# Kernel tuning notes

Measured on AMD Instinct MI355X. Metric: run time of the kernel, lower is better.

Reference implementation:

```python
import jax, jax.numpy as jnp
import numpy as np

D_MODEL = 4096
N_TYPES = 6  # fixed event_types list in the module


def setup_inputs() -> dict:
    key = jax.random.key(0)
    ks = jax.random.split(key, 7)
    E, B, d = 131072, 16384, D_MODEL
    return {
        "event_type": jax.random.randint(ks[0], (E,), 0, N_TYPES),
        "confidence": jax.random.uniform(ks[1], (E,), jnp.float32),
        "location": jax.random.uniform(ks[2], (E, 2), jnp.float32) * jnp.array([640.0, 480.0], jnp.float32),
        "batch_idx": jax.random.randint(ks[3], (E,), 0, B),
        "batch_size": B,
        "type_emb": jax.random.normal(ks[4], (N_TYPES, d // 4), jnp.float32),
        "W1": jax.random.normal(ks[5], (d // 2, d // 4 + 3), jnp.float32) / np.sqrt(d // 4 + 3).astype(np.float32),
        "b1": jnp.zeros((d // 2,), jnp.float32),
        "W2": jax.random.normal(ks[6], (d, d // 2), jnp.float32) / np.sqrt(d // 2).astype(np.float32),
        "b2": jnp.zeros((d,), jnp.float32),
    }


def reference(event_type, confidence, location, batch_idx, batch_size, type_emb, W1, b1, W2, b2):
    E = confidence.shape[0]
    B = batch_size
    # per-batch-slot max confidence (empty slots -> -inf)
    seg_max = jax.ops.segment_max(confidence, batch_idx, num_segments=B)
    is_top = confidence == seg_max[batch_idx]
    # first event attaining the max (matches torch's max-over-list semantics)
    cand = jnp.where(is_top, jnp.arange(E), E)
    top_idx = jnp.full((B,), E, dtype=cand.dtype).at[batch_idx].min(cand)
    has_event = top_idx < E
    safe_idx = jnp.where(has_event, top_idx, 0)

    emb = type_emb[event_type[safe_idx]]                 # [B, d/4]
    c = confidence[safe_idx][:, None]                    # [B, 1]
    loc = location[safe_idx] / jnp.array([640.0, 480.0], jnp.float32)  # [B, 2]
    feats = jnp.concatenate([emb, c, loc], axis=-1)      # [B, d/4 + 3]

    h = jax.nn.relu(feats @ W1.T + b1)                   # [B, d/2]
    out = h @ W2.T + b2                                  # [B, d]
    return jnp.where(has_event[:, None], out, jnp.zeros((), out.dtype))
```

## Files before the change

kernel.cpp:

```cpp
#include <hip/hip_runtime.h>
#include <hip/hip_bf16.h>

#define NT 6
#define BM 256
#define BN 256
#define BK 64
#define SLOT_S 32768
#define AH1 8192
#define BH0 16384
#define BH1 24576

typedef __attribute__((ext_vector_type(4))) float f32x4;
typedef __attribute__((ext_vector_type(8))) short bf16x8;

__device__ __forceinline__ short f2bf(float f) {
    __hip_bfloat16 h = __float2bfloat16(f);
    return (short)__builtin_bit_cast(unsigned short, h);
}

__global__ void k_segmax(const float* __restrict__ conf,
                         const int* __restrict__ bidx,
                         unsigned long long* __restrict__ packed, int E) {
    int i = blockIdx.x * blockDim.x + threadIdx.x;
    if (i >= E) return;
    unsigned cb = __float_as_uint(conf[i]);
    unsigned long long p = ((unsigned long long)cb << 32) | (unsigned)(~(unsigned)i);
    atomicMax(&packed[bidx[i]], p);
}

__global__ void k_base(const float* __restrict__ emb, const float* __restrict__ W1,
                       const float* __restrict__ b1, float* __restrict__ base,
                       float* __restrict__ vecs, int d2, int d4) {
    int gw = (blockIdx.x * blockDim.x + threadIdx.x) >> 6;
    int lane = threadIdx.x & 63;
    int t = gw / d2, n = gw % d2;
    const float* e = emb + (size_t)t * d4;
    const float* w = W1 + (size_t)n * (d4 + 3);
    float s = 0.f;
    for (int k = lane; k < d4; k += 64) s += e[k] * w[k];
#pragma unroll
    for (int m = 32; m; m >>= 1) s += __shfl_xor(s, m);
    if (lane == 0) {
        base[gw] = s + b1[n];
        if (t == 0) {
            vecs[n]          = w[d4];
            vecs[d2 + n]     = w[d4 + 1];
            vecs[2 * d2 + n] = w[d4 + 2];
        }
    }
}

__global__ void k_w2cast(const float* __restrict__ W2, short* __restrict__ W2b, long n) {
    long i = ((long)blockIdx.x * blockDim.x + threadIdx.x) * 8;
    if (i >= n) return;
    bf16x8 v;
#pragma unroll
    for (int j = 0; j < 8; ++j) v[j] = f2bf(W2[i + j]);
    *(bf16x8*)(W2b + i) = v;
}

__global__ void k_h(const unsigned long long* __restrict__ packed,
                    const int* __restrict__ etype, const float* __restrict__ loc,
                    const float* __restrict__ base, const float* __restrict__ vecs,
                    float* __restrict__ mask, short* __restrict__ h, int d2) {
    int b = blockIdx.x;
    int tid = threadIdx.x;
    unsigned long long p = packed[b];
    bool has = (p != 0ULL);
    float conf = 0.f, lx = 0.f, ly = 0.f;
    int t = 0;
    if (has) {
        unsigned idx = ~(unsigned)(p & 0xFFFFFFFFu);
        conf = __uint_as_float((unsigned)(p >> 32));
        t  = etype[idx];
        lx = loc[2 * (size_t)idx]     * (1.0f / 640.0f);
        ly = loc[2 * (size_t)idx + 1] * (1.0f / 480.0f);
    }
    if (tid == 0) mask[b] = has ? 1.0f : 0.0f;
    const float* bs = base + (size_t)t * d2;
    const float* cv = vecs;
    const float* xv = vecs + d2;
    const float* yv = vecs + 2 * d2;
    int n0 = tid * 8;
    bf16x8 v;
#pragma unroll
    for (int j = 0; j < 8; ++j) {
        int n = n0 + j;
        float g = bs[n] + conf * cv[n] + lx * xv[n] + ly * yv[n];
        g = fmaxf(g, 0.f);
        v[j] = has ? f2bf(g) : (short)0;
    }
    *(bf16x8*)(h + (size_t)b * d2 + n0) = v;
}


#define GLL(src, dst) __builtin_amdgcn_global_load_lds(                      \
    (const __attribute__((address_space(1))) void*)(src),                    \
    (__attribute__((address_space(3))) void*)(dst), 16, 0, 0)

#define ST_AH0(ws, kt) { GLL(pA + (size_t)(kt) * 64, (ws) + dst1);           \
                         GLL(pA + (size_t)64 * K + (kt) * 64, (ws) + dst2); }
#define ST_AH1(ws, kt) { GLL(pA + (size_t)128 * K + (kt) * 64, (ws) + AH1 + dst1); \
                         GLL(pA + (size_t)192 * K + (kt) * 64, (ws) + AH1 + dst2); }
#define ST_BH0(ws, kt) { GLL(pB + (size_t)(kt) * 64, (ws) + BH0 + dst1);     \
                         GLL(pB + (size_t)64 * K + (kt) * 64, (ws) + BH0 + dst2); }
#define ST_BH1(ws, kt) { GLL(pB + (size_t)128 * K + (kt) * 64, (ws) + BH1 + dst1); \
                         GLL(pB + (size_t)192 * K + (kt) * 64, (ws) + BH1 + dst2); }

__global__ __launch_bounds__(512, 2)
void k_gemm(const short* __restrict__ A, const short* __restrict__ Bm,
            const float* __restrict__ b2, const float* __restrict__ mask,
            float* __restrict__ C, int M, int N, int K, int nbn) {
    __shared__ __align__(16) short lds[2 * SLOT_S];

    int tid = threadIdx.x;
    int lane = tid & 63;
    int wave = tid >> 6;
    int wr = wave >> 2, wc = wave & 3;

    int bid = blockIdx.x;
    int wg = (bid & 7) * ((int)gridDim.x >> 3) + (bid >> 3);
    int bm = wg / nbn, bn = wg % nbn;
    int row0 = bm * BM, col0 = bn * BN;

    int r1 = tid >> 3;
    int pg = tid & 7;
    int cg = pg ^ (r1 & 7);
    const short* pA = A + (size_t)(row0 + r1) * K + cg * 8;
    const short* pB = Bm + (size_t)(col0 + r1) * K + cg * 8;
    int dst1 = tid * 8;
    int dst2 = 4096 + tid * 8;

    int frow = lane & 15, fk = lane >> 4;
    int kx = frow & 7;
    int aoffs0 = (wr * 64 + frow) * 64 + ((fk) ^ kx) * 8;
    int aoffs1 = (wr * 64 + frow) * 64 + ((4 + fk) ^ kx) * 8;
    int boffs0 = (wc * 32 + frow) * 64 + ((fk) ^ kx) * 8;
    int boffs1 = (wc * 32 + frow) * 64 + ((4 + fk) ^ kx) * 8;

    f32x4 acc[8][4] = {};
    bf16x8 aA[8][2], bB[4][2];

    int KT = K / BK;

    ST_AH0(lds, 0); ST_BH0(lds, 0); ST_BH1(lds, 0); ST_AH1(lds, 0);
    asm volatile("s_waitcnt vmcnt(0)" ::: "memory");
    __builtin_amdgcn_s_barrier();

#pragma unroll 1
    for (int t = 0; t < KT; ++t) {
        const short* sl = lds + (t & 1) * SLOT_S;
        short* wsl = lds + ((t + 1) & 1) * SLOT_S;

#pragma unroll
        for (int m = 0; m < 4; ++m) {
            aA[m][0]     = *(const bf16x8*)(sl + aoffs0 + m * 1024);
            aA[m][1]     = *(const bf16x8*)(sl + aoffs1 + m * 1024);
        }
#pragma unroll
        for (int n = 0; n < 2; ++n) {
            bB[n][0]     = *(const bf16x8*)(sl + BH0 + boffs0 + n * 1024);
            bB[n][1]     = *(const bf16x8*)(sl + BH0 + boffs1 + n * 1024);
            bB[2 + n][0] = *(const bf16x8*)(sl + BH1 + boffs0 + n * 1024);
            bB[2 + n][1] = *(const bf16x8*)(sl + BH1 + boffs1 + n * 1024);
        }
#pragma unroll
        for (int m = 0; m < 4; ++m) {
            aA[4 + m][0] = *(const bf16x8*)(sl + AH1 + aoffs0 + m * 1024);
            aA[4 + m][1] = *(const bf16x8*)(sl + AH1 + aoffs1 + m * 1024);
        }

        if (t < KT - 1) {
            ST_AH0(wsl, t + 1); ST_BH0(wsl, t + 1);
            ST_BH1(wsl, t + 1); ST_AH1(wsl, t + 1);
        }

        __builtin_amdgcn_s_setprio(1);
#pragma unroll
        for (int m = 0; m < 8; ++m)
#pragma unroll
            for (int n = 0; n < 4; ++n) {
                acc[m][n] = __builtin_amdgcn_mfma_f32_16x16x32_bf16(
                    aA[m][0], bB[n][0], acc[m][n], 0, 0, 0);
                acc[m][n] = __builtin_amdgcn_mfma_f32_16x16x32_bf16(
                    aA[m][1], bB[n][1], acc[m][n], 0, 0, 0);
            }
        __builtin_amdgcn_s_setprio(0);

        if (t < KT - 1) {
            asm volatile("s_waitcnt vmcnt(0)" ::: "memory");
            __builtin_amdgcn_s_barrier();
        }
    }

#pragma unroll
    for (int mi = 0; mi < 8; ++mi) {
        int rbase = row0 + (mi >> 2) * 128 + wr * 64 + (mi & 3) * 16 + fk * 4;
#pragma unroll
        for (int j = 0; j < 4; ++j) {
            int r = rbase + j;
            float mk = mask[r];
#pragma unroll
            for (int ni = 0; ni < 4; ++ni) {
                int cc = col0 + (ni >> 1) * 128 + wc * 32 + (ni & 1) * 16 + frow;
                C[(size_t)r * N + cc] = (acc[mi][ni][j] + b2[cc]) * mk;
            }
        }
    }
}

extern "C" void kernel_launch(void* const* d_in, const int* in_sizes, int n_in,
                              void* d_out, int out_size, void* d_ws, size_t ws_size,
                              hipStream_t stream) {
    const int* etype   = (const int*)d_in[0];
    const float* conf  = (const float*)d_in[1];
    const float* loc   = (const float*)d_in[2];
    const int* bidx    = (const int*)d_in[3];
    const float* emb   = (const float*)d_in[5];
    const float* W1    = (const float*)d_in[6];
    const float* b1    = (const float*)d_in[7];
    const float* W2    = (const float*)d_in[8];
    const float* b2    = (const float*)d_in[9];
    float* out = (float*)d_out;

    int E  = in_sizes[0];
    int d2 = in_sizes[7];
    int d  = in_sizes[9];
    int d4 = in_sizes[5] / NT;
    int B  = out_size / d;

    char* ws = (char*)d_ws;
    unsigned long long* packed = (unsigned long long*)ws;
    float* mask = (float*)(ws + (size_t)B * 8);
    float* base = mask + B;
    float* vecs = base + NT * d2;
    short* w2b  = (short*)(vecs + 3 * d2);
    short* h    = w2b + (size_t)d * d2;

    hipMemsetAsync(packed, 0, (size_t)B * 8, stream);
    k_segmax<<<(E + 255) / 256, 256, 0, stream>>>(conf, bidx, packed, E);
    k_base<<<(NT * d2) / 4, 256, 0, stream>>>(emb, W1, b1, base, vecs, d2, d4);
    long nw2 = (long)d * d2;
    k_w2cast<<<(int)(nw2 / 8 / 256), 256, 0, stream>>>(W2, w2b, nw2);
    k_h<<<B, 256, 0, stream>>>(packed, etype, loc, base, vecs, mask, h, d2);
    int nbm = B / BM, nbn = d / BN;
    k_gemm<<<dim3(nbm * nbn), dim3(512), 0, stream>>>(h, w2b, b2, mask, out, B, d, d2, nbn);
}
```

Baseline: 295.6 us.

## Load GEMM B fragments directly from global memory instead of staging through LDS

The B-operand tiles are no longer staged into shared memory. Each wave now reads its B fragments straight from global memory into registers every K step, which halves the LDS footprint and the LDS write/read traffic. In exchange, B loads are no longer shared across the waves in a row (the two row-waves load the same B data), global traffic per block rises, and the global loads are not prefetched ahead of the MFMAs, so their latency may stall compute.

```diff
diff --git a/kernel.cpp b/kernel.cpp
--- a/kernel.cpp
+++ b/kernel.cpp
@@ -5,10 +5,8 @@
 #define BM 256
 #define BN 256
 #define BK 64
-#define SLOT_S 32768
+#define SLOT_S 16384
 #define AH1 8192
-#define BH0 16384
-#define BH1 24576
 
 typedef __attribute__((ext_vector_type(4))) float f32x4;
 typedef __attribute__((ext_vector_type(8))) short bf16x8;
@@ -102,10 +100,6 @@
                          GLL(pA + (size_t)64 * K + (kt) * 64, (ws) + dst2); }
 #define ST_AH1(ws, kt) { GLL(pA + (size_t)128 * K + (kt) * 64, (ws) + AH1 + dst1); \
                          GLL(pA + (size_t)192 * K + (kt) * 64, (ws) + AH1 + dst2); }
-#define ST_BH0(ws, kt) { GLL(pB + (size_t)(kt) * 64, (ws) + BH0 + dst1);     \
-                         GLL(pB + (size_t)64 * K + (kt) * 64, (ws) + BH0 + dst2); }
-#define ST_BH1(ws, kt) { GLL(pB + (size_t)128 * K + (kt) * 64, (ws) + BH1 + dst1); \
-                         GLL(pB + (size_t)192 * K + (kt) * 64, (ws) + BH1 + dst2); }
 
 __global__ __launch_bounds__(512, 2)
 void k_gemm(const short* __restrict__ A, const short* __restrict__ Bm,
@@ -127,7 +121,6 @@
     int pg = tid & 7;
     int cg = pg ^ (r1 & 7);
     const short* pA = A + (size_t)(row0 + r1) * K + cg * 8;
-    const short* pB = Bm + (size_t)(col0 + r1) * K + cg * 8;
     int dst1 = tid * 8;
     int dst2 = 4096 + tid * 8;
 
@@ -135,15 +128,18 @@
     int kx = frow & 7;
     int aoffs0 = (wr * 64 + frow) * 64 + ((fk) ^ kx) * 8;
     int aoffs1 = (wr * 64 + frow) * 64 + ((4 + fk) ^ kx) * 8;
-    int boffs0 = (wc * 32 + frow) * 64 + ((fk) ^ kx) * 8;
-    int boffs1 = (wc * 32 + frow) * 64 + ((4 + fk) ^ kx) * 8;
+
+    const short* pB0 = Bm + (size_t)(col0 + wc * 32 + frow) * K + fk * 8;
+    const short* pB1 = pB0 + (size_t)16 * K;
+    const short* pB2 = pB0 + (size_t)128 * K;
+    const short* pB3 = pB0 + (size_t)144 * K;
 
     f32x4 acc[8][4] = {};
     bf16x8 aA[8][2], bB[4][2];
 
     int KT = K / BK;
 
-    ST_AH0(lds, 0); ST_BH0(lds, 0); ST_BH1(lds, 0); ST_AH1(lds, 0);
+    ST_AH0(lds, 0); ST_AH1(lds, 0);
     asm volatile("s_waitcnt vmcnt(0)" ::: "memory");
     __builtin_amdgcn_s_barrier();
 
@@ -151,6 +147,7 @@
     for (int t = 0; t < KT; ++t) {
         const short* sl = lds + (t & 1) * SLOT_S;
         short* wsl = lds + ((t + 1) & 1) * SLOT_S;
+        size_t ko = (size_t)t * 64;
 
 #pragma unroll
         for (int m = 0; m < 4; ++m) {
@@ -158,22 +155,20 @@
             aA[m][1]     = *(const bf16x8*)(sl + aoffs1 + m * 1024);
         }
 #pragma unroll
-        for (int n = 0; n < 2; ++n) {
-            bB[n][0]     = *(const bf16x8*)(sl + BH0 + boffs0 + n * 1024);
-            bB[n][1]     = *(const bf16x8*)(sl + BH0 + boffs1 + n * 1024);
-            bB[2 + n][0] = *(const bf16x8*)(sl + BH1 + boffs0 + n * 1024);
-            bB[2 + n][1] = *(const bf16x8*)(sl + BH1 + boffs1 + n * 1024);
-        }
-#pragma unroll
         for (int m = 0; m < 4; ++m) {
             aA[4 + m][0] = *(const bf16x8*)(sl + AH1 + aoffs0 + m * 1024);
             aA[4 + m][1] = *(const bf16x8*)(sl + AH1 + aoffs1 + m * 1024);
         }
 
-        if (t < KT - 1) {
-            ST_AH0(wsl, t + 1); ST_BH0(wsl, t + 1);
-            ST_BH1(wsl, t + 1); ST_AH1(wsl, t + 1);
-        }
+#pragma unroll
+        for (int ks = 0; ks < 2; ++ks) {
+            bB[0][ks] = *(const bf16x8*)(pB0 + ko + ks * 32);
+            bB[1][ks] = *(const bf16x8*)(pB1 + ko + ks * 32);
+            bB[2][ks] = *(const bf16x8*)(pB2 + ko + ks * 32);
+            bB[3][ks] = *(const bf16x8*)(pB3 + ko + ks * 32);
+        }
+
+        if (t < KT - 1) { ST_AH0(wsl, t + 1); ST_AH1(wsl, t + 1); }
 
         __builtin_amdgcn_s_setprio(1);
 #pragma unroll
```

Result: slower. 469.3 us (+58.8%).

## Switch GEMM inner loop to 32x32x16 MFMA with contiguous per-wave tiles

Applied to the files above, without the earlier changes.

Replaces the 16x16x32 bf16 MFMA tiling with 32x32x16 MFMA, so each wave owns a contiguous 128x64 output tile held in four-by-two 16-float accumulators. LDS fragment reads are re-indexed to keep the XOR swizzle, and the epilogue is rewritten for the 32x32 accumulator layout. The larger MFMA cuts instruction count and LDS fragment reads per FLOP, at the cost of a different register-pressure profile and a changed write pattern in the epilogue.

```diff
diff --git a/kernel.cpp b/kernel.cpp
--- a/kernel.cpp
+++ b/kernel.cpp
@@ -7,10 +7,10 @@
 #define BK 64
 #define SLOT_S 32768
 #define AH1 8192
-#define BH0 16384
+#define BOFF_A 16384
 #define BH1 24576
 
-typedef __attribute__((ext_vector_type(4))) float f32x4;
+typedef __attribute__((ext_vector_type(16))) float f32x16;
 typedef __attribute__((ext_vector_type(8))) short bf16x8;
 
 __device__ __forceinline__ short f2bf(float f) {
@@ -102,8 +102,8 @@
                          GLL(pA + (size_t)64 * K + (kt) * 64, (ws) + dst2); }
 #define ST_AH1(ws, kt) { GLL(pA + (size_t)128 * K + (kt) * 64, (ws) + AH1 + dst1); \
                          GLL(pA + (size_t)192 * K + (kt) * 64, (ws) + AH1 + dst2); }
-#define ST_BH0(ws, kt) { GLL(pB + (size_t)(kt) * 64, (ws) + BH0 + dst1);     \
-                         GLL(pB + (size_t)64 * K + (kt) * 64, (ws) + BH0 + dst2); }
+#define ST_BH0(ws, kt) { GLL(pB + (size_t)(kt) * 64, (ws) + BOFF_A + dst1);  \
+                         GLL(pB + (size_t)64 * K + (kt) * 64, (ws) + BOFF_A + dst2); }
 #define ST_BH1(ws, kt) { GLL(pB + (size_t)128 * K + (kt) * 64, (ws) + BH1 + dst1); \
                          GLL(pB + (size_t)192 * K + (kt) * 64, (ws) + BH1 + dst2); }
 
@@ -131,15 +131,16 @@
     int dst1 = tid * 8;
     int dst2 = 4096 + tid * 8;
 
-    int frow = lane & 15, fk = lane >> 4;
-    int kx = frow & 7;
-    int aoffs0 = (wr * 64 + frow) * 64 + ((fk) ^ kx) * 8;
-    int aoffs1 = (wr * 64 + frow) * 64 + ((4 + fk) ^ kx) * 8;
-    int boffs0 = (wc * 32 + frow) * 64 + ((fk) ^ kx) * 8;
-    int boffs1 = (wc * 32 + frow) * 64 + ((4 + fk) ^ kx) * 8;
-
-    f32x4 acc[8][4] = {};
-    bf16x8 aA[8][2], bB[4][2];
+    int l31 = lane & 31, kh = lane >> 5;
+    int kx7 = l31 & 7;
+    int aBase = (wr * 128 + l31) * 64;
+    int bBase = BOFF_A + (wc * 64 + l31) * 64;
+    int coff[4];
+#pragma unroll
+    for (int s = 0; s < 4; ++s) coff[s] = ((2 * s + kh) ^ kx7) * 8;
+
+    f32x16 acc[4][2] = {};
+    bf16x8 aA[4][4], bB[2][4];
 
     int KT = K / BK;
 
@@ -153,22 +154,15 @@
         short* wsl = lds + ((t + 1) & 1) * SLOT_S;
 
 #pragma unroll
-        for (int m = 0; m < 4; ++m) {
-            aA[m][0]     = *(const bf16x8*)(sl + aoffs0 + m * 1024);
-            aA[m][1]     = *(const bf16x8*)(sl + aoffs1 + m * 1024);
-        }
-#pragma unroll
-        for (int n = 0; n < 2; ++n) {
-            bB[n][0]     = *(const bf16x8*)(sl + BH0 + boffs0 + n * 1024);
-            bB[n][1]     = *(const bf16x8*)(sl + BH0 + boffs1 + n * 1024);
-            bB[2 + n][0] = *(const bf16x8*)(sl + BH1 + boffs0 + n * 1024);
-            bB[2 + n][1] = *(const bf16x8*)(sl + BH1 + boffs1 + n * 1024);
-        }
-#pragma unroll
-        for (int m = 0; m < 4; ++m) {
-            aA[4 + m][0] = *(const bf16x8*)(sl + AH1 + aoffs0 + m * 1024);
-            aA[4 + m][1] = *(const bf16x8*)(sl + AH1 + aoffs1 + m * 1024);
-        }
+        for (int mi = 0; mi < 4; ++mi)
+#pragma unroll
+            for (int s = 0; s < 4; ++s)
+                aA[mi][s] = *(const bf16x8*)(sl + aBase + mi * 2048 + coff[s]);
+#pragma unroll
+        for (int ni = 0; ni < 2; ++ni)
+#pragma unroll
+            for (int s = 0; s < 4; ++s)
+                bB[ni][s] = *(const bf16x8*)(sl + bBase + ni * 2048 + coff[s]);
 
         if (t < KT - 1) {
             ST_AH0(wsl, t + 1); ST_BH0(wsl, t + 1);
@@ -177,14 +171,13 @@
 
         __builtin_amdgcn_s_setprio(1);
 #pragma unroll
-        for (int m = 0; m < 8; ++m)
-#pragma unroll
-            for (int n = 0; n < 4; ++n) {
-                acc[m][n] = __builtin_amdgcn_mfma_f32_16x16x32_bf16(
-                    aA[m][0], bB[n][0], acc[m][n], 0, 0, 0);
-                acc[m][n] = __builtin_amdgcn_mfma_f32_16x16x32_bf16(
-                    aA[m][1], bB[n][1], acc[m][n], 0, 0, 0);
-            }
+        for (int mi = 0; mi < 4; ++mi)
+#pragma unroll
+            for (int ni = 0; ni < 2; ++ni)
+#pragma unroll
+                for (int s = 0; s < 4; ++s)
+                    acc[mi][ni] = __builtin_amdgcn_mfma_f32_32x32x16_bf16(
+                        aA[mi][s], bB[ni][s], acc[mi][ni], 0, 0, 0);
         __builtin_amdgcn_s_setprio(0);
 
         if (t < KT - 1) {
@@ -194,16 +187,19 @@
     }
 
 #pragma unroll
-    for (int mi = 0; mi < 8; ++mi) {
-        int rbase = row0 + (mi >> 2) * 128 + wr * 64 + (mi & 3) * 16 + fk * 4;
-#pragma unroll
-        for (int j = 0; j < 4; ++j) {
-            int r = rbase + j;
-            float mk = mask[r];
-#pragma unroll
-            for (int ni = 0; ni < 4; ++ni) {
-                int cc = col0 + (ni >> 1) * 128 + wc * 32 + (ni & 1) * 16 + frow;
-                C[(size_t)r * N + cc] = (acc[mi][ni][j] + b2[cc]) * mk;
+    for (int mi = 0; mi < 4; ++mi) {
+        int rb = row0 + wr * 128 + mi * 32 + 4 * kh;
+#pragma unroll
+        for (int q = 0; q < 4; ++q) {
+#pragma unroll
+            for (int j = 0; j < 4; ++j) {
+                int r = rb + 8 * q + j;
+                float mk = mask[r];
+#pragma unroll
+                for (int ni = 0; ni < 2; ++ni) {
+                    int c = col0 + wc * 64 + ni * 32 + l31;
+                    C[(size_t)r * N + c] = (acc[mi][ni][q * 4 + j] + b2[c]) * mk;
+                }
             }
         }
     }
```

New measurement: 330.9 us. 12.0% more time.
